# Optimization experiments

Measured on AMD Instinct MI355X. Metric: run time of the kernel, lower is better.

## Reference

```python
import jax, jax.numpy as jnp
import numpy as np

ATT_SCALE = 1.0  # att_scale_factor


def setup_inputs() -> dict:
    key = jax.random.key(0)
    k1, k2, k3, k4, k5 = jax.random.split(key, 5)
    B, P, IMG_D, SEQ_D, H = 64, 576, 1024, 1024, 512
    seq_features = jax.random.normal(k1, (B, SEQ_D), dtype=jnp.float32)
    img_features = jax.random.normal(k2, (B, P, IMG_D), dtype=jnp.float32)
    # torch nn.Linear weights: [out_features, in_features], scaled to typical init magnitude
    W_seq = jax.random.normal(k3, (H, SEQ_D), dtype=jnp.float32) * (1.0 / np.sqrt(SEQ_D))
    W_img = jax.random.normal(k4, (H, IMG_D), dtype=jnp.float32) * (1.0 / np.sqrt(IMG_D))
    W_w = jax.random.normal(k5, (1, H), dtype=jnp.float32) * (1.0 / np.sqrt(H))
    return {"seq_features": seq_features, "img_features": img_features,
            "W_seq": W_seq, "W_img": W_img, "W_w": W_w}


def reference(seq_features, img_features, W_seq, W_img, W_w):
    # tanh(SeqTrans(seq)) broadcast over patch dim (avoids explicit .repeat)
    seq_h = jnp.tanh(jnp.einsum('bd,hd->bh', seq_features, W_seq))          # [B, H]
    img_h = jnp.tanh(jnp.einsum('bpd,hd->bph', img_features, W_img))        # [B, P, H]
    attend = seq_h[:, None, :] * img_h                                       # [B, P, H]
    # Dropout is Identity (att_dropout=None)
    scores = ATT_SCALE * jnp.einsum('bph,oh->bpo', attend, W_w)              # [B, P, 1]
    alpha = jax.nn.softmax(scores, axis=1)                                   # softmax over patches
    # weighted sum over patches; alpha broadcasts over channel dim (no .repeat needed)
    attended_img = jnp.sum(img_features * alpha, axis=1)                     # [B, IMG_D]
    return attended_img
```

## Files before the change

### kernel.cpp

```cpp
#include <hip/hip_runtime.h>
#include <hip/hip_bf16.h>

#define BB 64
#define PP 576
#define DD 1024
#define HH 512

typedef __attribute__((ext_vector_type(4))) float f32x4;
typedef __attribute__((ext_vector_type(8))) short bf16x8;

__device__ __forceinline__ unsigned short f2bf(float f) {
    union { float f; unsigned u; } v; v.f = f;
    unsigned r = v.u + 0x7FFF + ((v.u >> 16) & 1);
    return (unsigned short)(r >> 16);
}

__device__ __forceinline__ float fast_tanh(float x) {
    float e = __expf(2.f * x);
    return 1.f - 2.f / (e + 1.f);
}

__device__ __forceinline__ void gload16(const void* g, void* l) {
    __builtin_amdgcn_global_load_lds((const __attribute__((address_space(1))) unsigned int*)g,
                                     (__attribute__((address_space(3))) unsigned int*)l,
                                     16, 0, 0);
}

__global__ __launch_bounds__(256) void k_convert(const float* __restrict__ w,
                                                 unsigned short* __restrict__ o) {
    int i = (blockIdx.x * 256 + threadIdx.x) * 4;
    f32x4 v = *(const f32x4*)(w + i);
    ushort4 r;
    r.x = f2bf(v.x); r.y = f2bf(v.y); r.z = f2bf(v.z); r.w = f2bf(v.w);
    *(ushort4*)(o + i) = r;
}

__global__ __launch_bounds__(128) void k_seq(const float* __restrict__ seq,
                                             const float* __restrict__ W_seq,
                                             const float* __restrict__ W_w,
                                             float* __restrict__ g) {
    int b = blockIdx.x;
    int h = blockIdx.y * 128 + threadIdx.x;
    __shared__ float s_seq[DD];
    #pragma unroll
    for (int i = 0; i < 8; i++) s_seq[threadIdx.x + i * 128] = seq[b * DD + threadIdx.x + i * 128];
    __syncthreads();
    const float* wr = W_seq + (size_t)h * DD;
    float acc = 0.f;
    #pragma unroll 4
    for (int d = 0; d < DD; d += 4) {
        f32x4 w4 = *(const f32x4*)(wr + d);
        acc += w4.x * s_seq[d] + w4.y * s_seq[d + 1] + w4.z * s_seq[d + 2] + w4.w * s_seq[d + 3];
    }
    g[b * HH + h] = fast_tanh(acc) * W_w[h];
}

__global__ __launch_bounds__(256) void k_scores(const float* __restrict__ img,
                                                const unsigned short* __restrict__ Wb,
                                                const float* __restrict__ g,
                                                float* __restrict__ sp) {
    int b = blockIdx.y;
    int rt = blockIdx.x % 9;
    int ch = blockIdx.x / 9;
    int p0 = rt * 64;
    int h0 = ch * 256;
    int tid = threadIdx.x;
    int w = tid >> 6, lane = tid & 63;

    __shared__ unsigned short As[64 * 64];
    __shared__ unsigned short Bs[256 * 64];
    __shared__ float gs[256];
    __shared__ float red[4][64];

    gs[tid] = g[b * HH + h0 + tid];

    f32x4 acc[4][4];
    #pragma unroll
    for (int m = 0; m < 4; m++)
        #pragma unroll
        for (int n = 0; n < 4; n++) acc[m][n] = (f32x4)0.f;

    int ar = tid >> 2;
    int ac = (tid & 3) * 16;
    const float* asrc = img + ((size_t)(b * PP + p0 + ar)) * DD + ac;
    int cp = (tid & 3) * 2;
    int aw0 = ar * 64 + ((cp ^ (ar & 7)) * 8);
    int aw1 = ar * 64 + (((cp + 1) ^ (ar & 7)) * 8);

    int brow_l = lane >> 3;
    int bchunk = lane & 7;

    for (int kr = 0; kr < 16; ++kr) {
        int k0 = kr * 64;
        if (kr) __syncthreads();
        #pragma unroll
        for (int i = 0; i < 8; ++i) {
            int hr = (w * 8 + i) * 8 + brow_l;
            const unsigned short* src = Wb + (size_t)(h0 + hr) * DD + k0 + ((bchunk ^ (hr & 7)) * 8);
            gload16(src, &Bs[(w * 8 + i) * 512]);
        }
        f32x4 v0 = *(const f32x4*)(asrc + k0);
        f32x4 v1 = *(const f32x4*)(asrc + k0 + 4);
        f32x4 v2 = *(const f32x4*)(asrc + k0 + 8);
        f32x4 v3 = *(const f32x4*)(asrc + k0 + 12);
        bf16x8 pa, pb;
        pa[0] = (short)f2bf(v0.x); pa[1] = (short)f2bf(v0.y);
        pa[2] = (short)f2bf(v0.z); pa[3] = (short)f2bf(v0.w);
        pa[4] = (short)f2bf(v1.x); pa[5] = (short)f2bf(v1.y);
        pa[6] = (short)f2bf(v1.z); pa[7] = (short)f2bf(v1.w);
        pb[0] = (short)f2bf(v2.x); pb[1] = (short)f2bf(v2.y);
        pb[2] = (short)f2bf(v2.z); pb[3] = (short)f2bf(v2.w);
        pb[4] = (short)f2bf(v3.x); pb[5] = (short)f2bf(v3.y);
        pb[6] = (short)f2bf(v3.z); pb[7] = (short)f2bf(v3.w);
        *(bf16x8*)&As[aw0] = pa;
        *(bf16x8*)&As[aw1] = pb;
        __syncthreads();

        #pragma unroll
        for (int ks = 0; ks < 2; ++ks) {
            int cbase = ks * 4 + (lane >> 4);
            bf16x8 af[4], bfv[4];
            #pragma unroll
            for (int m = 0; m < 4; ++m) {
                int row = m * 16 + (lane & 15);
                af[m] = *(const bf16x8*)&As[row * 64 + ((cbase ^ (row & 7)) * 8)];
            }
            #pragma unroll
            for (int n = 0; n < 4; ++n) {
                int hr = w * 64 + n * 16 + (lane & 15);
                bfv[n] = *(const bf16x8*)&Bs[hr * 64 + ((cbase ^ (hr & 7)) * 8)];
            }
            #pragma unroll
            for (int m = 0; m < 4; ++m)
                #pragma unroll
                for (int n = 0; n < 4; ++n)
                    acc[m][n] = __builtin_amdgcn_mfma_f32_16x16x32_bf16(af[m], bfv[n], acc[m][n], 0, 0, 0);
        }
    }

    float part[4][4];
    #pragma unroll
    for (int m = 0; m < 4; m++)
        #pragma unroll
        for (int j = 0; j < 4; j++) part[m][j] = 0.f;
    #pragma unroll
    for (int m = 0; m < 4; ++m)
        #pragma unroll
        for (int n = 0; n < 4; ++n) {
            float gv = gs[w * 64 + n * 16 + (lane & 15)];
            f32x4 v = acc[m][n];
            #pragma unroll
            for (int j = 0; j < 4; ++j) part[m][j] += fast_tanh(v[j]) * gv;
        }
    #pragma unroll
    for (int mask = 1; mask < 16; mask <<= 1)
        #pragma unroll
        for (int m = 0; m < 4; ++m)
            #pragma unroll
            for (int j = 0; j < 4; ++j)
                part[m][j] += __shfl_xor(part[m][j], mask, 64);
    if ((lane & 15) == 0) {
        int hi = lane >> 4;
        #pragma unroll
        for (int m = 0; m < 4; ++m)
            #pragma unroll
            for (int j = 0; j < 4; ++j)
                red[w][m * 16 + hi * 4 + j] = part[m][j];
    }
    __syncthreads();
    if (tid < 64) {
        float s = red[0][tid] + red[1][tid] + red[2][tid] + red[3][tid];
        sp[(size_t)ch * (BB * PP) + b * PP + p0 + tid] = s;
    }
}

__global__ __launch_bounds__(576) void k_softmax(const float* __restrict__ sp,
                                                 float* __restrict__ alpha) {
    int b = blockIdx.x;
    int t = threadIdx.x;
    __shared__ float red[9];
    float s = sp[b * PP + t] + sp[BB * PP + b * PP + t];
    float m = s;
    #pragma unroll
    for (int off = 32; off; off >>= 1) m = fmaxf(m, __shfl_xor(m, off, 64));
    int w = t >> 6;
    if ((t & 63) == 0) red[w] = m;
    __syncthreads();
    float gm = red[0];
    #pragma unroll
    for (int i = 1; i < 9; i++) gm = fmaxf(gm, red[i]);
    float e = __expf(s - gm);
    float sum = e;
    #pragma unroll
    for (int off = 32; off; off >>= 1) sum += __shfl_xor(sum, off, 64);
    __syncthreads();
    if ((t & 63) == 0) red[w] = sum;
    __syncthreads();
    float gsum = 0.f;
    #pragma unroll
    for (int i = 0; i < 9; i++) gsum += red[i];
    alpha[b * PP + t] = e / gsum;
}

__global__ __launch_bounds__(256) void k_attend(const float* __restrict__ img,
                                                const float* __restrict__ alpha,
                                                float* __restrict__ part) {
    int b = blockIdx.y;
    int pc = blockIdx.x;
    int t = threadIdx.x;
    __shared__ float al[64];
    if (t < 64) al[t] = alpha[b * PP + pc * 64 + t];
    __syncthreads();
    int d = t * 4;
    f32x4 acc = (f32x4)0.f;
    const float* base = img + ((size_t)b * PP + (size_t)pc * 64) * DD + d;
    #pragma unroll 4
    for (int i = 0; i < 64; i++) {
        f32x4 v = *(const f32x4*)(base + (size_t)i * DD);
        acc += al[i] * v;
    }
    float* o = part + ((size_t)pc * BB + b) * DD + d;
    *(f32x4*)o = acc;
}

__global__ __launch_bounds__(256) void k_reduce(const float* __restrict__ part,
                                                float* __restrict__ out) {
    int i = blockIdx.x * 256 + threadIdx.x;
    float s = 0.f;
    #pragma unroll
    for (int pc = 0; pc < 9; pc++) s += part[pc * (BB * DD) + i];
    out[i] = s;
}

extern "C" void kernel_launch(void* const* d_in, const int* in_sizes, int n_in,
                              void* d_out, int out_size, void* d_ws, size_t ws_size,
                              hipStream_t stream) {
    const float* seq   = (const float*)d_in[0];
    const float* img   = (const float*)d_in[1];
    const float* W_seq = (const float*)d_in[2];
    const float* W_img = (const float*)d_in[3];
    const float* W_w   = (const float*)d_in[4];
    float* out = (float*)d_out;

    char* ws = (char*)d_ws;
    unsigned short* Wb = (unsigned short*)ws;
    float* g      = (float*)(ws + 1048576);
    float* sp     = (float*)(ws + 1048576 + 131072);
    float* alpha  = (float*)(ws + 1048576 + 131072 + 294912);
    float* part   = (float*)(ws + 1048576 + 131072 + 294912 + 147456);

    k_convert<<<512, 256, 0, stream>>>(W_img, Wb);
    k_seq<<<dim3(BB, 4), 128, 0, stream>>>(seq, W_seq, W_w, g);
    k_scores<<<dim3(18, BB), 256, 0, stream>>>(img, Wb, g, sp);
    k_softmax<<<BB, 576, 0, stream>>>(sp, alpha);
    k_attend<<<dim3(9, BB), 256, 0, stream>>>(img, alpha, part);
    k_reduce<<<256, 256, 0, stream>>>(part, out);
}
```

Before: 124.3 us.

## Double-buffer A/B tiles in score GEMM to overlap loads with MFMA

The score kernel now keeps two LDS buffers for the image and weight tiles. It issues the next k-slice's async weight loads and global image loads before the MFMA work on the current slice, then packs A into the other buffer afterwards, so each iteration needs one barrier instead of two. The gate values move from shared memory into registers, and the reduction scratch reuses the A buffer. The cost is double the LDS footprint (about 40KB per block), which may lower occupancy, plus extra live registers for the prefetched A values.

```diff
diff --git a/kernel.cpp b/kernel.cpp
--- a/kernel.cpp
+++ b/kernel.cpp
@@ -67,12 +67,12 @@
     int tid = threadIdx.x;
     int w = tid >> 6, lane = tid & 63;
 
-    __shared__ unsigned short As[64 * 64];
-    __shared__ unsigned short Bs[256 * 64];
-    __shared__ float gs[256];
-    __shared__ float red[4][64];
-
-    gs[tid] = g[b * HH + h0 + tid];
+    __shared__ unsigned short As[2][64 * 64];
+    __shared__ unsigned short Bs[2][256 * 64];
+
+    float gr[4];
+    #pragma unroll
+    for (int n = 0; n < 4; ++n) gr[n] = g[b * HH + h0 + w * 64 + n * 16 + (lane & 15)];
 
     f32x4 acc[4][4];
     #pragma unroll
@@ -90,19 +90,16 @@
     int brow_l = lane >> 3;
     int bchunk = lane & 7;
 
-    for (int kr = 0; kr < 16; ++kr) {
+    auto stageB = [&](int bi, int kr) {
         int k0 = kr * 64;
-        if (kr) __syncthreads();
         #pragma unroll
         for (int i = 0; i < 8; ++i) {
             int hr = (w * 8 + i) * 8 + brow_l;
             const unsigned short* src = Wb + (size_t)(h0 + hr) * DD + k0 + ((bchunk ^ (hr & 7)) * 8);
-            gload16(src, &Bs[(w * 8 + i) * 512]);
-        }
-        f32x4 v0 = *(const f32x4*)(asrc + k0);
-        f32x4 v1 = *(const f32x4*)(asrc + k0 + 4);
-        f32x4 v2 = *(const f32x4*)(asrc + k0 + 8);
-        f32x4 v3 = *(const f32x4*)(asrc + k0 + 12);
+            gload16(src, &Bs[bi][(w * 8 + i) * 512]);
+        }
+    };
+    auto packA = [&](int bi, f32x4 v0, f32x4 v1, f32x4 v2, f32x4 v3) {
         bf16x8 pa, pb;
         pa[0] = (short)f2bf(v0.x); pa[1] = (short)f2bf(v0.y);
         pa[2] = (short)f2bf(v0.z); pa[3] = (short)f2bf(v0.w);
@@ -112,10 +109,31 @@
         pb[2] = (short)f2bf(v2.z); pb[3] = (short)f2bf(v2.w);
         pb[4] = (short)f2bf(v3.x); pb[5] = (short)f2bf(v3.y);
         pb[6] = (short)f2bf(v3.z); pb[7] = (short)f2bf(v3.w);
-        *(bf16x8*)&As[aw0] = pa;
-        *(bf16x8*)&As[aw1] = pb;
-        __syncthreads();
-
+        *(bf16x8*)&As[bi][aw0] = pa;
+        *(bf16x8*)&As[bi][aw1] = pb;
+    };
+
+    stageB(0, 0);
+    {
+        f32x4 v0 = *(const f32x4*)(asrc);
+        f32x4 v1 = *(const f32x4*)(asrc + 4);
+        f32x4 v2 = *(const f32x4*)(asrc + 8);
+        f32x4 v3 = *(const f32x4*)(asrc + 12);
+        packA(0, v0, v1, v2, v3);
+    }
+    __syncthreads();
+
+    f32x4 va0, va1, va2, va3;
+    for (int kr = 0; kr < 16; ++kr) {
+        int cur = kr & 1, nxt = cur ^ 1;
+        if (kr < 15) {
+            stageB(nxt, kr + 1);
+            int k0 = (kr + 1) * 64;
+            va0 = *(const f32x4*)(asrc + k0);
+            va1 = *(const f32x4*)(asrc + k0 + 4);
+            va2 = *(const f32x4*)(asrc + k0 + 8);
+            va3 = *(const f32x4*)(asrc + k0 + 12);
+        }
         #pragma unroll
         for (int ks = 0; ks < 2; ++ks) {
             int cbase = ks * 4 + (lane >> 4);
@@ -123,12 +141,12 @@
             #pragma unroll
             for (int m = 0; m < 4; ++m) {
                 int row = m * 16 + (lane & 15);
-                af[m] = *(const bf16x8*)&As[row * 64 + ((cbase ^ (row & 7)) * 8)];
+                af[m] = *(const bf16x8*)&As[cur][row * 64 + ((cbase ^ (row & 7)) * 8)];
             }
             #pragma unroll
             for (int n = 0; n < 4; ++n) {
                 int hr = w * 64 + n * 16 + (lane & 15);
-                bfv[n] = *(const bf16x8*)&Bs[hr * 64 + ((cbase ^ (hr & 7)) * 8)];
+                bfv[n] = *(const bf16x8*)&Bs[cur][hr * 64 + ((cbase ^ (hr & 7)) * 8)];
             }
             #pragma unroll
             for (int m = 0; m < 4; ++m)
@@ -136,6 +154,8 @@
                 for (int n = 0; n < 4; ++n)
                     acc[m][n] = __builtin_amdgcn_mfma_f32_16x16x32_bf16(af[m], bfv[n], acc[m][n], 0, 0, 0);
         }
+        if (kr < 15) packA(nxt, va0, va1, va2, va3);
+        __syncthreads();
     }
 
     float part[4][4];
@@ -147,7 +167,7 @@
     for (int m = 0; m < 4; ++m)
         #pragma unroll
         for (int n = 0; n < 4; ++n) {
-            float gv = gs[w * 64 + n * 16 + (lane & 15)];
+            float gv = gr[n];
             f32x4 v = acc[m][n];
             #pragma unroll
             for (int j = 0; j < 4; ++j) part[m][j] += fast_tanh(v[j]) * gv;
@@ -159,17 +179,19 @@
             #pragma unroll
             for (int j = 0; j < 4; ++j)
                 part[m][j] += __shfl_xor(part[m][j], mask, 64);
+
+    float* red = (float*)As;
     if ((lane & 15) == 0) {
         int hi = lane >> 4;
         #pragma unroll
         for (int m = 0; m < 4; ++m)
             #pragma unroll
             for (int j = 0; j < 4; ++j)
-                red[w][m * 16 + hi * 4 + j] = part[m][j];
+                red[w * 64 + m * 16 + hi * 4 + j] = part[m][j];
     }
     __syncthreads();
     if (tid < 64) {
-        float s = red[0][tid] + red[1][tid] + red[2][tid] + red[3][tid];
+        float s = red[tid] + red[64 + tid] + red[128 + tid] + red[192 + tid];
         sp[(size_t)ch * (BB * PP) + b * PP + p0 + tid] = s;
     }
 }
```

Result: slower. 152.3 us (+22.5%).
